# Optimization experiments

Measured on AMD Instinct MI355X. Metric: run time of the kernel, lower is better.

## Reference

```python
import jax, jax.numpy as jnp
import numpy as np


def setup_inputs() -> dict:
    key = jax.random.key(0)
    k1, k2 = jax.random.split(key)
    x = jax.random.normal(k1, (32, 512, 512, 1), dtype=jnp.float32)
    se = jnp.ones((3, 3), dtype=jnp.float32)
    rank = jax.random.normal(k2, (9,), dtype=jnp.float32)
    return {"x": x, "se": se, "rank": rank}


def _extract_patches_3x3_same(x):
    # x: [B, H, W, 1] -> [B, H, W, 9], zero-padded SAME, row-major window order
    B, H, W, C = x.shape
    xp = jnp.pad(x, ((0, 0), (1, 1), (1, 1), (0, 0)))
    shifts = [xp[:, dy:dy + H, dx:dx + W, 0] for dy in range(3) for dx in range(3)]
    return jnp.stack(shifts, axis=-1)  # [B, H, W, 9]


def reference(x, se, rank):
    # Faithful to Morph2D.call: patches * se, sort ascending over the 9-window,
    # softmax(rank)-weighted sum -> soft rank-order filter.
    patches = _extract_patches_3x3_same(x)              # [B,H,W,9]
    weighted = patches * se.reshape(9)                  # elementwise by SE
    sorted_p = jnp.sort(weighted, axis=-1)              # ascending over window
    w = jax.nn.softmax(rank)                            # [9]
    out = jnp.sum(sorted_p * w, axis=-1)                # [B,H,W]
    return out.reshape(x.shape)                         # [B,H,W,1]
```

## Files before the change

kernel.cpp:

```cpp
#include <hip/hip_runtime.h>


#define HH 512
#define WW 512

#define RFL(x) __int_as_float(__builtin_amdgcn_readfirstlane(__float_as_int(x)))
#define CSWAP(a,b) { float lo_ = fminf(v[a], v[b]); float hi_ = fmaxf(v[a], v[b]); v[a] = lo_; v[b] = hi_; }

__global__ __launch_bounds__(256, 8) void morph2d_kernel(
    const float* __restrict__ x, const float* __restrict__ se9,
    const float* __restrict__ rank, float* __restrict__ out)
{
    int nper = gridDim.x >> 3;
    int lb   = (blockIdx.x & 7) * nper + (blockIdx.x >> 3);
    int g    = lb * 256 + threadIdx.x;

    int gx = g & 127;
    int y  = (g >> 7) & 511;
    int b  = g >> 16;
    int x4 = gx << 2;

    const float* img = x + (size_t)b * (HH * WW);
    int offL = max(x4 - 1, 0);
    int offR = min(x4 + 4, WW - 1);

    float rv[3][6];
    if (y > 0 && y < HH - 1) {
        const float* p = img + (y - 1) * WW;
        #pragma unroll
        for (int r = 0; r < 3; ++r) {
            float4 c = *(const float4*)(p + x4);
            float lf = p[offL];
            float rt = p[offR];
            rv[r][0] = lf;  rv[r][1] = c.x; rv[r][2] = c.y;
            rv[r][3] = c.z; rv[r][4] = c.w; rv[r][5] = rt;
            p += WW;
        }
    } else {
        #pragma unroll
        for (int r = 0; r < 3; ++r) {
            int ry  = y - 1 + r;
            int ryc = min(max(ry, 0), HH - 1);
            const float* p = img + ryc * WW;
            float  m = (ry >= 0 && ry < HH) ? 1.f : 0.f;
            float4 c = *(const float4*)(p + x4);
            rv[r][0] = p[offL] * m; rv[r][1] = c.x * m; rv[r][2] = c.y * m;
            rv[r][3] = c.z * m;     rv[r][4] = c.w * m; rv[r][5] = p[offR] * m;
        }
    }

    float w[9], se[9];
    float inv_s;
    {
        float s = 0.f;
        float e[9];
        #pragma unroll
        for (int i = 0; i < 9; ++i) { e[i] = __expf(rank[i]); s += e[i]; }
        inv_s = RFL(1.0f / s);
        #pragma unroll
        for (int i = 0; i < 9; ++i) { w[i] = RFL(e[i]); se[i] = RFL(se9[i]); }
    }

    #pragma unroll
    for (int r = 0; r < 3; ++r) {
        rv[r][0] = (x4 == 0)       ? 0.f : rv[r][0];
        rv[r][5] = (x4 + 4 >= WW)  ? 0.f : rv[r][5];
    }

    float4 res;
    float* resp = &res.x;
    #pragma unroll
    for (int j = 0; j < 4; ++j) {
        float v[9];
        #pragma unroll
        for (int dy = 0; dy < 3; ++dy) {
            v[dy*3+0] = rv[dy][j]   * se[dy*3+0];
            v[dy*3+1] = rv[dy][j+1] * se[dy*3+1];
            v[dy*3+2] = rv[dy][j+2] * se[dy*3+2];
        }
        CSWAP(0,3) CSWAP(1,7) CSWAP(2,5) CSWAP(4,8)
        CSWAP(0,7) CSWAP(2,4) CSWAP(3,8) CSWAP(5,6)
        CSWAP(0,2) CSWAP(1,3) CSWAP(4,5) CSWAP(7,8)
        CSWAP(1,4) CSWAP(3,6) CSWAP(5,7)
        CSWAP(0,1) CSWAP(2,4) CSWAP(3,5) CSWAP(6,8)
        CSWAP(2,3) CSWAP(4,5) CSWAP(6,7)
        CSWAP(1,2) CSWAP(3,4) CSWAP(5,6)

        float acc = 0.f;
        #pragma unroll
        for (int i = 0; i < 9; ++i) acc = fmaf(v[i], w[i], acc);
        resp[j] = acc * inv_s;
    }

    *(float4*)(out + (((size_t)b * HH + y) * WW + x4)) = res;
}

extern "C" void kernel_launch(void* const* d_in, const int* in_sizes, int n_in,
                              void* d_out, int out_size, void* d_ws, size_t ws_size,
                              hipStream_t stream) {
    const float* x    = (const float*)d_in[0];
    const float* se   = (const float*)d_in[1];
    const float* rank = (const float*)d_in[2];
    float* out = (float*)d_out;

    const int total_threads = 32 * HH * (WW / 4);
    morph2d_kernel<<<total_threads / 256, 256, 0, stream>>>(x, se, rank, out);
}
```

Baseline: 96.58 us.

## Compute a 4x4 output tile per thread to reuse loaded rows

Each thread now produces four consecutive output rows of four pixels, loading six input rows instead of three per output row. This cuts redundant row loads and per-thread setup such as the softmax, exp and broadcast work, and launches a quarter as many threads. The softmax normalisation is folded into the weights and the weighted sum becomes a tree reduction. Launch bounds drop to allow more registers, at the cost of lower occupancy and fewer blocks to hide latency.

```diff
diff --git a/kernel.cpp b/kernel.cpp
--- a/kernel.cpp
+++ b/kernel.cpp
@@ -6,8 +6,16 @@
 
 #define RFL(x) __int_as_float(__builtin_amdgcn_readfirstlane(__float_as_int(x)))
 #define CSWAP(a,b) { float lo_ = fminf(v[a], v[b]); float hi_ = fmaxf(v[a], v[b]); v[a] = lo_; v[b] = hi_; }
+#define SORT9 \
+    CSWAP(0,3) CSWAP(1,7) CSWAP(2,5) CSWAP(4,8) \
+    CSWAP(0,7) CSWAP(2,4) CSWAP(3,8) CSWAP(5,6) \
+    CSWAP(0,2) CSWAP(1,3) CSWAP(4,5) CSWAP(7,8) \
+    CSWAP(1,4) CSWAP(3,6) CSWAP(5,7) \
+    CSWAP(0,1) CSWAP(2,4) CSWAP(3,5) CSWAP(6,8) \
+    CSWAP(2,3) CSWAP(4,5) CSWAP(6,7) \
+    CSWAP(1,2) CSWAP(3,4) CSWAP(5,6)
 
-__global__ __launch_bounds__(256, 8) void morph2d_kernel(
+__global__ __launch_bounds__(256, 4) void morph2d_kernel(
     const float* __restrict__ x, const float* __restrict__ se9,
     const float* __restrict__ rank, float* __restrict__ out)
 {
@@ -16,83 +24,83 @@
     int g    = lb * 256 + threadIdx.x;
 
     int gx = g & 127;
-    int y  = (g >> 7) & 511;
-    int b  = g >> 16;
+    int rg = (g >> 7) & 127;
+    int b  = g >> 14;
     int x4 = gx << 2;
+    int y0 = rg << 2;
 
     const float* img = x + (size_t)b * (HH * WW);
     int offL = max(x4 - 1, 0);
     int offR = min(x4 + 4, WW - 1);
 
-    float rv[3][6];
-    if (y > 0 && y < HH - 1) {
-        const float* p = img + (y - 1) * WW;
-        #pragma unroll
-        for (int r = 0; r < 3; ++r) {
-            float4 c = *(const float4*)(p + x4);
-            float lf = p[offL];
-            float rt = p[offR];
-            rv[r][0] = lf;  rv[r][1] = c.x; rv[r][2] = c.y;
-            rv[r][3] = c.z; rv[r][4] = c.w; rv[r][5] = rt;
-            p += WW;
-        }
-    } else {
-        #pragma unroll
-        for (int r = 0; r < 3; ++r) {
-            int ry  = y - 1 + r;
-            int ryc = min(max(ry, 0), HH - 1);
-            const float* p = img + ryc * WW;
-            float  m = (ry >= 0 && ry < HH) ? 1.f : 0.f;
-            float4 c = *(const float4*)(p + x4);
-            rv[r][0] = p[offL] * m; rv[r][1] = c.x * m; rv[r][2] = c.y * m;
-            rv[r][3] = c.z * m;     rv[r][4] = c.w * m; rv[r][5] = p[offR] * m;
-        }
+    float R[6][6];
+
+    #pragma unroll
+    for (int r = 1; r <= 4; ++r) {
+        const float* p = img + (y0 - 1 + r) * WW;
+        float4 c = *(const float4*)(p + x4);
+        R[r][0] = p[offL]; R[r][1] = c.x; R[r][2] = c.y;
+        R[r][3] = c.z;     R[r][4] = c.w; R[r][5] = p[offR];
+    }
+    {
+        int ry = y0 - 1;
+        const float* p = img + max(ry, 0) * WW;
+        float4 c = *(const float4*)(p + x4);
+        float  m = (ry >= 0) ? 1.f : 0.f;
+        R[0][0] = p[offL] * m; R[0][1] = c.x * m; R[0][2] = c.y * m;
+        R[0][3] = c.z * m;     R[0][4] = c.w * m; R[0][5] = p[offR] * m;
+    }
+    {
+        int ry = y0 + 4;
+        const float* p = img + min(ry, HH - 1) * WW;
+        float4 c = *(const float4*)(p + x4);
+        float  m = (ry < HH) ? 1.f : 0.f;
+        R[5][0] = p[offL] * m; R[5][1] = c.x * m; R[5][2] = c.y * m;
+        R[5][3] = c.z * m;     R[5][4] = c.w * m; R[5][5] = p[offR] * m;
     }
 
-    float w[9], se[9];
-    float inv_s;
+    float w0,w1,w2,w3,w4,w5,w6,w7,w8;
+    float s0,s1,s2,s3,s4,s5,s6,s7,s8;
     {
-        float s = 0.f;
-        float e[9];
+        float e[9]; float s = 0.f;
         #pragma unroll
         for (int i = 0; i < 9; ++i) { e[i] = __expf(rank[i]); s += e[i]; }
-        inv_s = RFL(1.0f / s);
-        #pragma unroll
-        for (int i = 0; i < 9; ++i) { w[i] = RFL(e[i]); se[i] = RFL(se9[i]); }
+        float inv = 1.0f / s;
+        w0=RFL(e[0]*inv); w1=RFL(e[1]*inv); w2=RFL(e[2]*inv);
+        w3=RFL(e[3]*inv); w4=RFL(e[4]*inv); w5=RFL(e[5]*inv);
+        w6=RFL(e[6]*inv); w7=RFL(e[7]*inv); w8=RFL(e[8]*inv);
+        s0=RFL(se9[0]); s1=RFL(se9[1]); s2=RFL(se9[2]); s3=RFL(se9[3]);
+        s4=RFL(se9[4]); s5=RFL(se9[5]); s6=RFL(se9[6]); s7=RFL(se9[7]); s8=RFL(se9[8]);
+    }
+
+    bool xl = (x4 == 0);
+    bool xr = (x4 + 4 >= WW);
+    #pragma unroll
+    for (int r = 0; r < 6; ++r) {
+        R[r][0] = xl ? 0.f : R[r][0];
+        R[r][5] = xr ? 0.f : R[r][5];
     }
 
     #pragma unroll
-    for (int r = 0; r < 3; ++r) {
-        rv[r][0] = (x4 == 0)       ? 0.f : rv[r][0];
-        rv[r][5] = (x4 + 4 >= WW)  ? 0.f : rv[r][5];
+    for (int r = 0; r < 4; ++r) {
+        float res[4];
+        #pragma unroll
+        for (int j = 0; j < 4; ++j) {
+            float v[9];
+            v[0] = R[r  ][j]*s0; v[1] = R[r  ][j+1]*s1; v[2] = R[r  ][j+2]*s2;
+            v[3] = R[r+1][j]*s3; v[4] = R[r+1][j+1]*s4; v[5] = R[r+1][j+2]*s5;
+            v[6] = R[r+2][j]*s6; v[7] = R[r+2][j+1]*s7; v[8] = R[r+2][j+2]*s8;
+            SORT9
+            float d0 = fmaf(v[0], w0, v[1]*w1);
+            float d1 = fmaf(v[2], w2, v[3]*w3);
+            float d2 = fmaf(v[4], w4, v[5]*w5);
+            float d3 = fmaf(v[6], w6, v[7]*w7);
+            float d4 = v[8]*w8;
+            res[j] = (d0 + d1) + (d2 + d3) + d4;
+        }
+        float4 o = { res[0], res[1], res[2], res[3] };
+        *(float4*)(out + (((size_t)b * HH + (y0 + r)) * WW + x4)) = o;
     }
-
-    float4 res;
-    float* resp = &res.x;
-    #pragma unroll
-    for (int j = 0; j < 4; ++j) {
-        float v[9];
-        #pragma unroll
-        for (int dy = 0; dy < 3; ++dy) {
-            v[dy*3+0] = rv[dy][j]   * se[dy*3+0];
-            v[dy*3+1] = rv[dy][j+1] * se[dy*3+1];
-            v[dy*3+2] = rv[dy][j+2] * se[dy*3+2];
-        }
-        CSWAP(0,3) CSWAP(1,7) CSWAP(2,5) CSWAP(4,8)
-        CSWAP(0,7) CSWAP(2,4) CSWAP(3,8) CSWAP(5,6)
-        CSWAP(0,2) CSWAP(1,3) CSWAP(4,5) CSWAP(7,8)
-        CSWAP(1,4) CSWAP(3,6) CSWAP(5,7)
-        CSWAP(0,1) CSWAP(2,4) CSWAP(3,5) CSWAP(6,8)
-        CSWAP(2,3) CSWAP(4,5) CSWAP(6,7)
-        CSWAP(1,2) CSWAP(3,4) CSWAP(5,6)
-
-        float acc = 0.f;
-        #pragma unroll
-        for (int i = 0; i < 9; ++i) acc = fmaf(v[i], w[i], acc);
-        resp[j] = acc * inv_s;
-    }
-
-    *(float4*)(out + (((size_t)b * HH + y) * WW + x4)) = res;
 }
 
 extern "C" void kernel_launch(void* const* d_in, const int* in_sizes, int n_in,
@@ -103,6 +111,6 @@
     const float* rank = (const float*)d_in[2];
     float* out = (float*)d_out;
 
-    const int total_threads = 32 * HH * (WW / 4);
+    const int total_threads = 32 * (HH / 4) * (WW / 4);
     morph2d_kernel<<<total_threads / 256, 256, 0, stream>>>(x, se, rank, out);
 }
```

Result: no change. 96.36 us (-0.2%).
